# Kernel tuning notes

Hardware: AMD Instinct MI355X
Metric: run time of the kernel (lower is better)

Reference implementation:

```python
import jax, jax.numpy as jnp
import numpy as np

DIM = 1024
NUM_HEADS = 16
HEAD_DIM = DIM // NUM_HEADS  # 64
T = 4096
ATTN_SCALE = 0.12


def _rope_tables(t, head_dim):
    # angular_freq: (1/1024)**linspace(0,1,head_dim//4), then zeros for head_dim//4 -> head_dim//2
    af = (1.0 / 1024.0) ** jnp.linspace(0.0, 1.0, head_dim // 4, dtype=jnp.float32)
    af = jnp.concatenate([af, jnp.zeros(head_dim // 4, dtype=jnp.float32)])
    theta = jnp.arange(t, dtype=jnp.float32)[:, None] * af[None, :]  # [T, head_dim//2]
    return jnp.cos(theta), jnp.sin(theta)


def _rms_norm(x):
    eps = jnp.finfo(jnp.float32).eps
    ms = jnp.mean(jnp.square(x.astype(jnp.float32)), axis=-1, keepdims=True)
    return (x * jax.lax.rsqrt(ms + eps)).astype(x.dtype)


def _rotary(x, cos, sin):
    # x: [B, T, H, D]; cos/sin: [T, D//2]
    xf = x.astype(jnp.float32)
    x1, x2 = jnp.split(xf, 2, axis=-1)
    c = cos[None, :, None, :]
    s = sin[None, :, None, :]
    y1 = x1 * c + x2 * s
    y2 = -x1 * s + x2 * c
    return jnp.concatenate([y1, y2], axis=-1).astype(x.dtype)


def setup_inputs() -> dict:
    key = jax.random.key(0)
    k1, k2, k3, k4 = jax.random.split(key, 4)
    std = 0.5 * DIM ** (-0.5)
    bound = (3.0 ** 0.5) * std
    x = jax.random.normal(k1, (1, T, DIM), dtype=jnp.float32)
    ve = jax.random.normal(k2, (1, T, DIM), dtype=jnp.float32)
    qkv_w = jax.random.uniform(k3, (3, DIM, DIM), dtype=jnp.float32, minval=-bound, maxval=bound)
    lambdas = jnp.array([0.5, 0.5], dtype=jnp.float32)
    # source zero-inits c_proj; use random weights for a non-degenerate baseline
    c_proj_w = jax.random.uniform(k4, (DIM, DIM), dtype=jnp.float32, minval=-bound, maxval=bound)
    return {"x": x, "ve": ve, "qkv_w": qkv_w, "lambdas": lambdas, "c_proj_w": c_proj_w}


def reference(x, ve, qkv_w, lambdas, c_proj_w):
    B, t, _ = x.shape
    # fused QKV: F.linear(x, qkv_w.flatten(end_dim=1)) -> [B, T, 3*dim]
    qkv = jnp.einsum('btd,ed->bte', x, qkv_w.reshape(3 * DIM, DIM))
    qkv = qkv.reshape(B, t, 3 * NUM_HEADS, HEAD_DIM)
    q, k, v = jnp.split(qkv, 3, axis=-2)  # each [B, T, H, Dh]
    # lambda-weighted value-embedding mix
    v = lambdas[0] * v + lambdas[1] * ve.reshape(B, t, NUM_HEADS, HEAD_DIM)
    # RMSNorm per head, then RoPE
    q, k = _rms_norm(q), _rms_norm(k)
    cos, sin = _rope_tables(t, HEAD_DIM)
    q, k = _rotary(q, cos, sin), _rotary(k, cos, sin)
    # causal attention with fixed scale (flex_attention w/ causal block mask)
    scores = jnp.einsum('bqhd,bkhd->bhqk', q, k) * ATTN_SCALE
    causal = jnp.tril(jnp.ones((t, t), dtype=bool))
    scores = jnp.where(causal[None, None], scores, jnp.finfo(scores.dtype).min)
    probs = jax.nn.softmax(scores, axis=-1)
    y = jnp.einsum('bhqk,bkhd->bqhd', probs, v).reshape(B, t, DIM)
    return jnp.einsum('btd,ed->bte', y, c_proj_w)
```

## Files before the change

### kernel.cpp

```cpp
#include <hip/hip_runtime.h>
#include <stdint.h>


typedef __attribute__((ext_vector_type(8))) __bf16 bf16x8;
typedef __attribute__((ext_vector_type(8))) unsigned short u16x8;
typedef __attribute__((ext_vector_type(4))) float f32x4;
typedef __attribute__((ext_vector_type(16))) float f32x16;

union U8 { u16x8 s; bf16x8 b; };
union PF { unsigned int u[4]; u16x8 s; bf16x8 b; };

__device__ __forceinline__ float bf2f(unsigned short u) {
  union { unsigned int i; float f; } c; c.i = ((unsigned int)u) << 16; return c.f;
}
__device__ __forceinline__ unsigned short f2bf(float f) {
  union { __bf16 h; unsigned short u; } c; c.h = (__bf16)f; return c.u;
}
__device__ __forceinline__ unsigned int pk2(float lo, float hi) {
  return (unsigned int)f2bf(lo) | ((unsigned int)f2bf(hi) << 16);
}

#define GLOAD16(gp, lp)                                                         \
  __builtin_amdgcn_global_load_lds(                                             \
      (const __attribute__((address_space(1))) void*)(gp),                      \
      (__attribute__((address_space(3))) void*)(lp), 16, 0, 0)

#define MFMA16(a, b, c) __builtin_amdgcn_mfma_f32_16x16x32_bf16((a), (b), (c), 0, 0, 0)
#define MFMA32(a, b, c) __builtin_amdgcn_mfma_f32_32x32x16_bf16((a), (b), (c), 0, 0, 0)

constexpr float ATTN_SCALE = 0.12f;
constexpr float LOG2E = 1.44269504088896340736f;
constexpr float QSCALE = ATTN_SCALE * LOG2E;

__global__ void rope_tab(float* __restrict__ ct, float* __restrict__ st) {
  const int i = blockIdx.x * 256 + threadIdx.x;
  if (i >= 4096 * 32) return;
  const int tt = i >> 5, k = i & 31;
  float cv = 1.0f, sv = 0.0f;
  if (k < 16) {
    const float af = powf(1.0f / 1024.0f, (float)k * (1.0f / 15.0f));
    const float th = (float)tt * af;
    cv = cosf(th);
    sv = sinf(th);
  }
  ct[i] = cv; st[i] = sv;
}

__global__ void cast_f2b8(const float* __restrict__ in, unsigned short* __restrict__ out, int n8) {
  const int i = blockIdx.x * 256 + threadIdx.x;
  if (i >= n8) return;
  const float4 a = ((const float4*)in)[2 * i];
  const float4 b = ((const float4*)in)[2 * i + 1];
  u16x8 o;
  o[0] = f2bf(a.x); o[1] = f2bf(a.y); o[2] = f2bf(a.z); o[3] = f2bf(a.w);
  o[4] = f2bf(b.x); o[5] = f2bf(b.y); o[6] = f2bf(b.z); o[7] = f2bf(b.w);
  ((u16x8*)out)[i] = o;
}

template <int OUT_BF16>
__global__ __launch_bounds__(256) void gemm_bt(
    const unsigned short* __restrict__ A, const unsigned short* __restrict__ B,
    void* __restrict__ Cout, int M, int N, int K) {
  __shared__ unsigned short lA[128 * 32];
  __shared__ unsigned short lB[128 * 32];
  const int nbn = N >> 7;
  const int bm = blockIdx.x / nbn, bn = blockIdx.x % nbn;
  const int t = threadIdx.x;
  const int w = t >> 6, l = t & 63;
  const int g = l >> 4, c = l & 15;
  const int wr = (w >> 1) * 64, wc = (w & 1) * 64;

  const int srow = t >> 2;
  const int scol = ((t & 3) << 4) ^ ((srow & 3) << 4);
  const char* ga = (const char*)(A + (size_t)(bm * 128 + srow) * K) + scol;
  const char* gb = (const char*)(B + (size_t)(bn * 128 + srow) * K) + scol;
  const size_t rowK2 = (size_t)64 * K * 2;
  char* la_dst = (char*)lA + t * 16;
  char* lb_dst = (char*)lB + t * 16;

  f32x4 acc[4][4] = {};

  for (int kt = 0; kt < K; kt += 32) {
    const char* gak = ga + (size_t)kt * 2;
    const char* gbk = gb + (size_t)kt * 2;
    GLOAD16(gak, la_dst);
    GLOAD16(gak + rowK2, la_dst + 4096);
    GLOAD16(gbk, lb_dst);
    GLOAD16(gbk + rowK2, lb_dst + 4096);
    __syncthreads();
    U8 af[4], bfr[4];
#pragma unroll
    for (int mi = 0; mi < 4; ++mi) {
      const int row = wr + 16 * mi + c;
      af[mi].s = *(const u16x8*)((const char*)lA + row * 64 + ((16 * g) ^ ((row & 3) << 4)));
    }
#pragma unroll
    for (int ni = 0; ni < 4; ++ni) {
      const int row = wc + 16 * ni + c;
      bfr[ni].s = *(const u16x8*)((const char*)lB + row * 64 + ((16 * g) ^ ((row & 3) << 4)));
    }
#pragma unroll
    for (int mi = 0; mi < 4; ++mi)
#pragma unroll
      for (int ni = 0; ni < 4; ++ni)
        acc[mi][ni] = MFMA16(af[mi].b, bfr[ni].b, acc[mi][ni]);
    __syncthreads();
  }
#pragma unroll
  for (int mi = 0; mi < 4; ++mi) {
#pragma unroll
    for (int ni = 0; ni < 4; ++ni) {
#pragma unroll
      for (int r = 0; r < 4; ++r) {
        const int row = bm * 128 + wr + 16 * mi + 4 * g + r;
        const int col = bn * 128 + wc + 16 * ni + c;
        const float v = acc[mi][ni][r];
        if (OUT_BF16)
          ((unsigned short*)Cout)[(size_t)row * N + col] = f2bf(v);
        else
          ((float*)Cout)[(size_t)row * N + col] = v;
      }
    }
  }
}

__device__ __forceinline__ void load64f(const unsigned short* p, float* x) {
#pragma unroll
  for (int j = 0; j < 8; ++j) {
    const u16x8 v = *(const u16x8*)(p + 8 * j);
#pragma unroll
    for (int e = 0; e < 8; ++e) x[8 * j + e] = bf2f(v[e]);
  }
}

__device__ __forceinline__ void rmsrope_store_blk(const float* x, const float* ct,
                                                  const float* st, unsigned short* outp,
                                                  float pscale) {
  float ms = 0.f;
#pragma unroll
  for (int j = 0; j < 64; ++j) ms += x[j] * x[j];
  const float sc = rsqrtf(ms * (1.0f / 64.0f) + 1.1920928955078125e-7f) * pscale;
  float y[64];
#pragma unroll
  for (int j = 0; j < 32; ++j) {
    const float cc = ct[j], ss = st[j];
    const float a = x[j] * sc, b = x[j + 32] * sc;
    y[j] = a * cc + b * ss;
    y[j + 32] = b * cc - a * ss;
  }
#pragma unroll
  for (int j = 0; j < 8; ++j) {
    u16x8 o;
#pragma unroll
    for (int e = 0; e < 8; ++e) o[e] = f2bf(y[8 * j + e]);
    *(u16x8*)(outp + 256 * j) = o;
  }
}

__global__ __launch_bounds__(256) void fuse_qkv(
    const unsigned short* __restrict__ qkv,
    const float* __restrict__ ve,
    const float* __restrict__ lam,
    const float* __restrict__ ct, const float* __restrict__ st,
    unsigned short* __restrict__ Qb,
    unsigned short* __restrict__ Kb,
    unsigned short* __restrict__ Vm)
{
  const int gid = blockIdx.x * 256 + threadIdx.x;
  const int h = gid >> 12, tt = gid & 4095;
  const unsigned short* base = qkv + (size_t)tt * 3072 + h * 64;
  const float* ctp = ct + tt * 32;
  const float* stp = st + tt * 32;
  const size_t blk = (size_t)h * 262144 + (tt >> 5) * 2048 + (tt & 31) * 8;
  float x[64];
  load64f(base, x);
  rmsrope_store_blk(x, ctp, stp, Qb + blk, QSCALE);
  load64f(base + 1024, x);
  rmsrope_store_blk(x, ctp, stp, Kb + blk, 1.0f);
  const float l0 = lam[0], l1 = lam[1];
  const float* vp = ve + (size_t)tt * 1024 + h * 64;
  load64f(base + 2048, x);
  unsigned short* vo = Vm + ((size_t)h * 4096 + tt) * 64;
#pragma unroll
  for (int j = 0; j < 8; ++j) {
    u16x8 o;
#pragma unroll
    for (int e = 0; e < 8; ++e) o[e] = f2bf(l0 * x[8 * j + e] + l1 * vp[8 * j + e]);
    *(u16x8*)(vo + 8 * j) = o;
  }
}

__global__ __launch_bounds__(256) void transpose_v(const unsigned short* __restrict__ vin,
                                                   unsigned short* __restrict__ vout) {
  __shared__ unsigned short tile[64][66];
  const int h = (int)(blockIdx.x & 15), tb = (int)(blockIdx.x >> 4);
  const int t = threadIdx.x;
  const int r = t >> 2, c0 = (t & 3) * 16;
  const unsigned short* src = vin + ((size_t)h * 4096 + tb * 64 + r) * 64 + c0;
#pragma unroll
  for (int j = 0; j < 16; ++j) tile[c0 + j][r] = src[j];
  __syncthreads();
#pragma unroll
  for (int s = 0; s < 2; ++s) {
    const int rr = (t >> 6) & 3;
    const int ll = t & 63;
    const int hh = ll >> 5, qq = ll & 31;
    const int d = qq + 32 * (rr & 1);
    const int kvc = 32 * s + 16 * (rr >> 1) + 8 * hh;
    const u16x8 v = *(const u16x8*)&tile[d][kvc];
    *(u16x8*)(vout + (size_t)h * 262144 + (2 * tb + s) * 2048 + rr * 512 + hh * 256 + qq * 8) = v;
  }
}

__global__ __launch_bounds__(256, 4) void attn_fa(
    const unsigned short* __restrict__ Qb,
    const unsigned short* __restrict__ Kb,
    const unsigned short* __restrict__ Vb,
    unsigned short* __restrict__ Y)
{
  __shared__ float oL[4][64][33];
  __shared__ float mlL[4][2][32];

  const int b = (int)blockIdx.x;
  const int h = 2 * (b & 7) + ((b >> 3) & 1);
  const int qb = 127 - (b >> 4);
  const int q0 = qb * 32;
  const int t = threadIdx.x;
  const int w = t >> 6, l = t & 63;
  const int lq = l & 31;
  const int hi = l >> 5;

  const unsigned short* kh = Kb + (size_t)h * 262144 + l * 8;
  const unsigned short* vh = Vb + (size_t)h * 262144 + l * 8;

  U8 qf[4];
  {
    const unsigned short* qp = Qb + (size_t)h * 262144 + qb * 2048 + l * 8;
#pragma unroll
    for (int dd = 0; dd < 4; ++dd) qf[dd].s = *(const u16x8*)(qp + dd * 512);
  }

  f32x16 o0 = {}, o1 = {};
  float osum = 0.0f, m = -3e38f;

  for (int ti = w; ti <= qb; ti += 4) {
    const unsigned short* kp = kh + ti * 2048;
    const unsigned short* vp = vh + ti * 2048;
    U8 kf[4], vf[4];
#pragma unroll
    for (int dd = 0; dd < 4; ++dd) kf[dd].s = *(const u16x8*)(kp + dd * 512);
#pragma unroll
    for (int r = 0; r < 4; ++r) vf[r].s = *(const u16x8*)(vp + r * 512);

    __builtin_amdgcn_s_setprio(1);
    f32x16 s0 = {};
#pragma unroll
    for (int dd = 0; dd < 4; ++dd) s0 = MFMA32(kf[dd].b, qf[dd].b, s0);
    __builtin_amdgcn_s_setprio(0);

    if (ti == qb) {
      const int thr0 = lq - 4 * hi;
#pragma unroll
      for (int e = 0; e < 16; ++e) {
        const int kvr = (e & 3) + 8 * (e >> 2);
        if (kvr > thr0) s0[e] = -3e38f;
      }
    }

    float pm;
    {
      float t0 = fmaxf(s0[0], s0[1]), t1 = fmaxf(s0[2], s0[3]);
      float t2 = fmaxf(s0[4], s0[5]), t3 = fmaxf(s0[6], s0[7]);
      float t4 = fmaxf(s0[8], s0[9]), t5 = fmaxf(s0[10], s0[11]);
      float t6 = fmaxf(s0[12], s0[13]), t7 = fmaxf(s0[14], s0[15]);
      pm = fmaxf(fmaxf(fmaxf(t0, t1), fmaxf(t2, t3)),
                 fmaxf(fmaxf(t4, t5), fmaxf(t6, t7)));
    }
    pm = fmaxf(pm, __shfl_xor(pm, 32));
    if (!__all(pm <= m + 8.0f)) {
      const float mn = fmaxf(m, pm);
      const float alpha = exp2f(m - mn);
#pragma unroll
      for (int e = 0; e < 16; ++e) { o0[e] *= alpha; o1[e] *= alpha; }
      osum *= alpha;
      m = mn;
    }
#pragma unroll
    for (int e = 0; e < 16; ++e) s0[e] = exp2f(s0[e] - m);
    {
      const float a0 = (s0[0] + s0[1]) + (s0[2] + s0[3]);
      const float a1 = (s0[4] + s0[5]) + (s0[6] + s0[7]);
      const float a2 = (s0[8] + s0[9]) + (s0[10] + s0[11]);
      const float a3 = (s0[12] + s0[13]) + (s0[14] + s0[15]);
      float rs = (a0 + a1) + (a2 + a3);
      rs += __shfl_xor(rs, 32);
      osum += rs;
    }

#define DO_SLAB(KS)                                                              \
  do {                                                                           \
    const unsigned int ua = pk2(s0[8 * (KS) + 0], s0[8 * (KS) + 1]);             \
    const unsigned int ub = pk2(s0[8 * (KS) + 2], s0[8 * (KS) + 3]);             \
    const unsigned int uc = pk2(s0[8 * (KS) + 4], s0[8 * (KS) + 5]);             \
    const unsigned int ud = pk2(s0[8 * (KS) + 6], s0[8 * (KS) + 7]);             \
    const unsigned int sa = (unsigned int)__shfl_xor((int)ua, 32);               \
    const unsigned int sb = (unsigned int)__shfl_xor((int)ub, 32);               \
    const unsigned int sc = (unsigned int)__shfl_xor((int)uc, 32);               \
    const unsigned int sd = (unsigned int)__shfl_xor((int)ud, 32);               \
    PF pf;                                                                       \
    pf.u[0] = hi ? sc : ua;                                                      \
    pf.u[1] = hi ? sd : ub;                                                      \
    pf.u[2] = hi ? uc : sa;                                                      \
    pf.u[3] = hi ? ud : sb;                                                      \
    __builtin_amdgcn_s_setprio(1);                                               \
    o0 = MFMA32(vf[2 * (KS)].b, pf.b, o0);                                       \
    o1 = MFMA32(vf[2 * (KS) + 1].b, pf.b, o1);                                   \
    __builtin_amdgcn_s_setprio(0);                                               \
  } while (0)

    DO_SLAB(0);
    DO_SLAB(1);
#undef DO_SLAB
  }

#pragma unroll
  for (int e = 0; e < 16; ++e) {
    const int d = (e & 3) + 8 * (e >> 2) + 4 * hi;
    oL[w][d][lq] = o0[e];
    oL[w][d + 32][lq] = o1[e];
  }
  if (hi == 0) { mlL[w][0][lq] = m; mlL[w][1][lq] = osum; }
  __syncthreads();

  const int q = t >> 3, dblk = t & 7;
  const float m0 = mlL[0][0][q], m1 = mlL[1][0][q];
  const float m2 = mlL[2][0][q], m3 = mlL[3][0][q];
  const float mm = fmaxf(fmaxf(m0, m1), fmaxf(m2, m3));
  const float f0 = exp2f(m0 - mm), f1 = exp2f(m1 - mm);
  const float f2 = exp2f(m2 - mm), f3 = exp2f(m3 - mm);
  const float den = f0 * mlL[0][1][q] + f1 * mlL[1][1][q] +
                    f2 * mlL[2][1][q] + f3 * mlL[3][1][q];
  const float invd = 1.0f / den;
  u16x8 yv;
#pragma unroll
  for (int i = 0; i < 8; ++i) {
    const int d = dblk * 8 + i;
    const float a = f0 * oL[0][d][q] + f1 * oL[1][d][q] +
                    f2 * oL[2][d][q] + f3 * oL[3][d][q];
    yv[i] = f2bf(a * invd);
  }
  *(u16x8*)(Y + (size_t)(q0 + q) * 1024 + h * 64 + dblk * 8) = yv;
}

extern "C" void kernel_launch(void* const* d_in, const int* in_sizes, int n_in,
                              void* d_out, int out_size, void* d_ws, size_t ws_size,
                              hipStream_t stream) {
  const float* x   = (const float*)d_in[0];
  const float* ve  = (const float*)d_in[1];
  const float* qw  = (const float*)d_in[2];
  const float* lam = (const float*)d_in[3];
  const float* pw  = (const float*)d_in[4];
  float* out = (float*)d_out;

  unsigned short* ws = (unsigned short*)d_ws;
  unsigned short* x_bf  = ws;
  unsigned short* wqkv  = x_bf + (size_t)4096 * 1024;
  unsigned short* wproj = wqkv + (size_t)3072 * 1024;
  unsigned short* qkv   = wproj + (size_t)1024 * 1024;
  unsigned short* Qb    = qkv + (size_t)4096 * 3072;
  unsigned short* Kb    = Qb + (size_t)4096 * 1024;
  unsigned short* Vm    = Kb + (size_t)4096 * 1024;
  unsigned short* Vb    = Vm + (size_t)4096 * 1024;
  unsigned short* Yb    = Vb + (size_t)4096 * 1024;
  float* ct = (float*)(Yb + (size_t)4096 * 1024);
  float* st = ct + 4096 * 32;

  rope_tab<<<512, 256, 0, stream>>>(ct, st);
  cast_f2b8<<<2048, 256, 0, stream>>>(x, x_bf, 524288);
  cast_f2b8<<<1536, 256, 0, stream>>>(qw, wqkv, 393216);
  cast_f2b8<<<512, 256, 0, stream>>>(pw, wproj, 131072);
  gemm_bt<1><<<768, 256, 0, stream>>>(x_bf, wqkv, (void*)qkv, 4096, 3072, 1024);
  fuse_qkv<<<256, 256, 0, stream>>>(qkv, ve, lam, ct, st, Qb, Kb, Vm);
  transpose_v<<<1024, 256, 0, stream>>>(Vm, Vb);
  attn_fa<<<2048, 256, 0, stream>>>(Qb, Kb, Vb, Yb);
  gemm_bt<0><<<256, 256, 0, stream>>>(Yb, wproj, (void*)out, 4096, 1024, 1024);
}
```

Before: 173.8 us.

## Fuse V transpose into fuse_qkv and compute softmax row sums via MFMA

The V mix is now written through a shared-memory tile inside fuse_qkv, which stores directly in the blocked transposed layout the attention kernel reads. This removes the separate transpose_v kernel and its intermediate buffer round trip. In the attention loop, the scalar row-sum reduction (adds plus a cross-lane shuffle) is replaced by an extra MFMA against a ones vector. This moves that work onto the matrix unit but adds one MFMA per slab and 16 accumulator registers, which may raise register pressure.

```diff
diff --git a/kernel.cpp b/kernel.cpp
--- a/kernel.cpp
+++ b/kernel.cpp
@@ -164,51 +164,45 @@
     const float* __restrict__ ct, const float* __restrict__ st,
     unsigned short* __restrict__ Qb,
     unsigned short* __restrict__ Kb,
-    unsigned short* __restrict__ Vm)
+    unsigned short* __restrict__ Vb)
 {
-  const int gid = blockIdx.x * 256 + threadIdx.x;
-  const int h = gid >> 12, tt = gid & 4095;
+  __shared__ unsigned short vtile[8][32][65];
+  const int b = (int)blockIdx.x;
+  const int h = b & 15, tg = b >> 4;
+  const int t = threadIdx.x;
+  const int g = t >> 5, lq = t & 31;
+  const int ti = tg * 8 + g;
+  const int tt = ti * 32 + lq;
+
   const unsigned short* base = qkv + (size_t)tt * 3072 + h * 64;
   const float* ctp = ct + tt * 32;
   const float* stp = st + tt * 32;
-  const size_t blk = (size_t)h * 262144 + (tt >> 5) * 2048 + (tt & 31) * 8;
+  const size_t blk = (size_t)h * 262144 + (size_t)ti * 2048 + lq * 8;
+
   float x[64];
   load64f(base, x);
   rmsrope_store_blk(x, ctp, stp, Qb + blk, QSCALE);
   load64f(base + 1024, x);
   rmsrope_store_blk(x, ctp, stp, Kb + blk, 1.0f);
+
   const float l0 = lam[0], l1 = lam[1];
   const float* vp = ve + (size_t)tt * 1024 + h * 64;
   load64f(base + 2048, x);
-  unsigned short* vo = Vm + ((size_t)h * 4096 + tt) * 64;
-#pragma unroll
-  for (int j = 0; j < 8; ++j) {
-    u16x8 o;
-#pragma unroll
-    for (int e = 0; e < 8; ++e) o[e] = f2bf(l0 * x[8 * j + e] + l1 * vp[8 * j + e]);
-    *(u16x8*)(vo + 8 * j) = o;
-  }
-}
-
-__global__ __launch_bounds__(256) void transpose_v(const unsigned short* __restrict__ vin,
-                                                   unsigned short* __restrict__ vout) {
-  __shared__ unsigned short tile[64][66];
-  const int h = (int)(blockIdx.x & 15), tb = (int)(blockIdx.x >> 4);
-  const int t = threadIdx.x;
-  const int r = t >> 2, c0 = (t & 3) * 16;
-  const unsigned short* src = vin + ((size_t)h * 4096 + tb * 64 + r) * 64 + c0;
-#pragma unroll
-  for (int j = 0; j < 16; ++j) tile[c0 + j][r] = src[j];
+#pragma unroll
+  for (int j = 0; j < 64; ++j) vtile[g][lq][j] = f2bf(l0 * x[j] + l1 * vp[j]);
   __syncthreads();
-#pragma unroll
-  for (int s = 0; s < 2; ++s) {
-    const int rr = (t >> 6) & 3;
-    const int ll = t & 63;
-    const int hh = ll >> 5, qq = ll & 31;
-    const int d = qq + 32 * (rr & 1);
-    const int kvc = 32 * s + 16 * (rr >> 1) + 8 * hh;
-    const u16x8 v = *(const u16x8*)&tile[d][kvc];
-    *(u16x8*)(vout + (size_t)h * 262144 + (2 * tb + s) * 2048 + rr * 512 + hh * 256 + qq * 8) = v;
+
+  unsigned short* vo = Vb + (size_t)h * 262144 + (size_t)ti * 2048 + lq * 8;
+#pragma unroll
+  for (int r = 0; r < 4; ++r) {
+    const int d = lq + 32 * (r & 1);
+#pragma unroll
+    for (int hi = 0; hi < 2; ++hi) {
+      u16x8 o;
+#pragma unroll
+      for (int j = 0; j < 8; ++j) o[j] = vtile[g][16 * (r >> 1) + 8 * hi + j][d];
+      *(u16x8*)(vo + r * 512 + hi * 256) = o;
+    }
   }
 }
 
@@ -240,8 +234,13 @@
     for (int dd = 0; dd < 4; ++dd) qf[dd].s = *(const u16x8*)(qp + dd * 512);
   }
 
+  U8 onesf;
+#pragma unroll
+  for (int e = 0; e < 8; ++e) onesf.s[e] = 0x3F80;
+
   f32x16 o0 = {}, o1 = {};
-  float osum = 0.0f, m = -3e38f;
+  f32x16 osum = {};
+  float m = -3e38f;
 
   for (int ti = w; ti <= qb; ti += 4) {
     const unsigned short* kp = kh + ti * 2048;
@@ -282,20 +281,11 @@
       const float alpha = exp2f(m - mn);
 #pragma unroll
       for (int e = 0; e < 16; ++e) { o0[e] *= alpha; o1[e] *= alpha; }
-      osum *= alpha;
+      osum[0] *= alpha;
       m = mn;
     }
 #pragma unroll
     for (int e = 0; e < 16; ++e) s0[e] = exp2f(s0[e] - m);
-    {
-      const float a0 = (s0[0] + s0[1]) + (s0[2] + s0[3]);
-      const float a1 = (s0[4] + s0[5]) + (s0[6] + s0[7]);
-      const float a2 = (s0[8] + s0[9]) + (s0[10] + s0[11]);
-      const float a3 = (s0[12] + s0[13]) + (s0[14] + s0[15]);
-      float rs = (a0 + a1) + (a2 + a3);
-      rs += __shfl_xor(rs, 32);
-      osum += rs;
-    }
 
 #define DO_SLAB(KS)                                                              \
   do {                                                                           \
@@ -315,6 +305,7 @@
     __builtin_amdgcn_s_setprio(1);                                               \
     o0 = MFMA32(vf[2 * (KS)].b, pf.b, o0);                                       \
     o1 = MFMA32(vf[2 * (KS) + 1].b, pf.b, o1);                                   \
+    osum = MFMA32(onesf.b, pf.b, osum);                                          \
     __builtin_amdgcn_s_setprio(0);                                               \
   } while (0)
 
@@ -329,7 +320,7 @@
     oL[w][d][lq] = o0[e];
     oL[w][d + 32][lq] = o1[e];
   }
-  if (hi == 0) { mlL[w][0][lq] = m; mlL[w][1][lq] = osum; }
+  if (hi == 0) { mlL[w][0][lq] = m; mlL[w][1][lq] = osum[0]; }
   __syncthreads();
 
   const int q = t >> 3, dblk = t & 7;
@@ -369,8 +360,7 @@
   unsigned short* qkv   = wproj + (size_t)1024 * 1024;
   unsigned short* Qb    = qkv + (size_t)4096 * 3072;
   unsigned short* Kb    = Qb + (size_t)4096 * 1024;
-  unsigned short* Vm    = Kb + (size_t)4096 * 1024;
-  unsigned short* Vb    = Vm + (size_t)4096 * 1024;
+  unsigned short* Vb    = Kb + (size_t)4096 * 1024;
   unsigned short* Yb    = Vb + (size_t)4096 * 1024;
   float* ct = (float*)(Yb + (size_t)4096 * 1024);
   float* st = ct + 4096 * 32;
@@ -380,8 +370,7 @@
   cast_f2b8<<<1536, 256, 0, stream>>>(qw, wqkv, 393216);
   cast_f2b8<<<512, 256, 0, stream>>>(pw, wproj, 131072);
   gemm_bt<1><<<768, 256, 0, stream>>>(x_bf, wqkv, (void*)qkv, 4096, 3072, 1024);
-  fuse_qkv<<<256, 256, 0, stream>>>(qkv, ve, lam, ct, st, Qb, Kb, Vm);
-  transpose_v<<<1024, 256, 0, stream>>>(Vm, Vb);
+  fuse_qkv<<<256, 256, 0, stream>>>(qkv, ve, lam, ct, st, Qb, Kb, Vb);
   attn_fa<<<2048, 256, 0, stream>>>(Qb, Kb, Vb, Yb);
   gemm_bt<0><<<256, 256, 0, stream>>>(Yb, wproj, (void*)out, 4096, 1024, 1024);
 }
```

After: 167.6 us. 3.6% less time.
